# Kernel optimization log

Hardware: AMD Instinct MI355X
Metric: run time of the kernel (lower is better)

The kernel has to match this reference:

```python
import jax, jax.numpy as jnp
import numpy as np

NQ = 4
DIM = 1 << NQ  # 16 statevector amplitudes

def _cnot_perm(c, t):
    idx = np.arange(DIM)
    cbit = (idx >> (NQ - 1 - c)) & 1
    return np.where(cbit == 1, idx ^ (1 << (NQ - 1 - t)), idx)

# BasicEntanglerLayers CNOT ring: (0,1),(1,2),(2,3),(3,0)
CNOT_PERMS = [jnp.asarray(_cnot_perm(q, (q + 1) % NQ)) for q in range(NQ)]
_idx = np.arange(DIM)
SIGNS = jnp.asarray(np.stack([1.0 - 2.0 * ((_idx >> (NQ - 1 - q)) & 1) for q in range(NQ)]).astype(np.float32))  # (NQ, DIM), PauliZ eigenvalues


def _apply_rx(state, theta, q):
    """Apply RX(theta) on wire q. state: (N, DIM) complex64. theta: scalar or (N,)."""
    half = theta * 0.5
    c = jnp.cos(half).astype(jnp.complex64)
    js = (1j * jnp.sin(half)).astype(jnp.complex64)
    if jnp.ndim(theta) == 1:
        c = c[:, None, None]
        js = js[:, None, None]
    d1, d2 = 1 << q, 1 << (NQ - 1 - q)
    st = state.reshape(-1, d1, 2, d2)
    a0, a1 = st[:, :, 0, :], st[:, :, 1, :]
    out = jnp.stack([c * a0 - js * a1, c * a1 - js * a0], axis=2)
    return out.reshape(state.shape)


def circuit(angles, weights):
    """AngleEmbedding(RX) + BasicEntanglerLayers(RX + CNOT ring) + <Z_i>.
    angles: (N, NQ) real. weights: (L, NQ). returns (N, NQ)."""
    N = angles.shape[0]
    state = jnp.zeros((N, DIM), jnp.complex64).at[:, 0].set(1.0)
    for q in range(NQ):  # AngleEmbedding: per-sample RX angles
        state = _apply_rx(state, angles[:, q], q)
    for l in range(weights.shape[0]):  # entangler layers (static count)
        for q in range(NQ):
            state = _apply_rx(state, weights[l, q], q)
        for q in range(NQ):
            state = state[:, CNOT_PERMS[q]]
    probs = jnp.real(state) ** 2 + jnp.imag(state) ** 2
    return probs @ SIGNS.T


def setup_inputs() -> dict:
    key = jax.random.key(0)
    ks = jax.random.split(key, 5)
    B, S = 32, 2048
    TWO_PI = 6.2831853
    return {
        "x": jax.random.normal(ks[0], (B, S, NQ), jnp.float32),
        "weights_Q": jax.random.uniform(ks[1], (1, NQ), jnp.float32) * TWO_PI,
        "weights_K": jax.random.uniform(ks[2], (1, NQ), jnp.float32) * TWO_PI,
        "weights_V": jax.random.uniform(ks[3], (1, NQ), jnp.float32) * TWO_PI,
        "weights_C": jax.random.uniform(ks[4], (1, NQ), jnp.float32) * TWO_PI,
    }


def reference(x, weights_Q, weights_K, weights_V, weights_C):
    B, S, E = x.shape  # E == NQ == 4
    flat = x.reshape(B * S, E)
    Q = circuit(flat, weights_Q).reshape(B, S, E)
    K = circuit(flat, weights_K).reshape(B, S, E)
    V = circuit(flat, weights_V).reshape(B, S, E)
    scores = jnp.einsum('bqe,bke->bqk', Q, K) / (E ** 0.5)
    attn = jax.nn.softmax(scores, axis=-1)
    ctx = jnp.einsum('bqk,bke->bqe', attn, V)
    return circuit(ctx.reshape(B * S, E), weights_C).reshape(B, S, E)
```

## Files before the change

### kernel.cpp

```cpp
#include <hip/hip_runtime.h>

#define DIM 16
#define SEQ 2048


template<int P>
__device__ __forceinline__ void rx_bit(float sr[DIM], float si[DIM], float ch, float sh) {
    constexpr int m = 1 << P;
    #pragma unroll
    for (int i = 0; i < DIM; ++i) {
        if ((i & m) == 0) {
            const int j = i | m;
            float r0 = sr[i], i0 = si[i], r1 = sr[j], i1 = si[j];
            sr[i] = fmaf(ch, r0,  sh * i1);
            si[i] = fmaf(ch, i0, -sh * r1);
            sr[j] = fmaf(ch, r1,  sh * i0);
            si[j] = fmaf(ch, i1, -sh * r0);
        }
    }
}

template<int PC, int PT>
__device__ __forceinline__ void cnot_g(float sr[DIM], float si[DIM]) {
    constexpr int cm = 1 << PC, tm = 1 << PT;
    #pragma unroll
    for (int i = 0; i < DIM; ++i) {
        if ((i & cm) && !(i & tm)) {
            const int j = i | tm;
            float t;
            t = sr[i]; sr[i] = sr[j]; sr[j] = t;
            t = si[i]; si[i] = si[j]; si[j] = t;
        }
    }
}

__device__ __forceinline__ void embed(float sr[DIM], float si[DIM], float4 a) {
    #pragma unroll
    for (int i = 0; i < DIM; ++i) { sr[i] = 0.f; si[i] = 0.f; }
    sr[0] = 1.f;
    float ch, sh;
    __sincosf(0.5f * a.x, &sh, &ch); rx_bit<3>(sr, si, ch, sh);
    __sincosf(0.5f * a.y, &sh, &ch); rx_bit<2>(sr, si, ch, sh);
    __sincosf(0.5f * a.z, &sh, &ch); rx_bit<1>(sr, si, ch, sh);
    __sincosf(0.5f * a.w, &sh, &ch); rx_bit<0>(sr, si, ch, sh);
}

__device__ __forceinline__ void layer(float sr[DIM], float si[DIM], float4 w) {
    float ch, sh;
    __sincosf(0.5f * w.x, &sh, &ch); rx_bit<3>(sr, si, ch, sh);
    __sincosf(0.5f * w.y, &sh, &ch); rx_bit<2>(sr, si, ch, sh);
    __sincosf(0.5f * w.z, &sh, &ch); rx_bit<1>(sr, si, ch, sh);
    __sincosf(0.5f * w.w, &sh, &ch); rx_bit<0>(sr, si, ch, sh);
    cnot_g<3,2>(sr, si);
    cnot_g<2,1>(sr, si);
    cnot_g<1,0>(sr, si);
    cnot_g<0,3>(sr, si);
}

__device__ __forceinline__ float4 measure(const float sr[DIM], const float si[DIM]) {
    float e0 = 0.f, e1 = 0.f, e2 = 0.f, e3 = 0.f;
    #pragma unroll
    for (int i = 0; i < DIM; ++i) {
        float p = fmaf(sr[i], sr[i], si[i] * si[i]);
        e0 += (i & 8) ? -p : p;
        e1 += (i & 4) ? -p : p;
        e2 += (i & 2) ? -p : p;
        e3 += (i & 1) ? -p : p;
    }
    return make_float4(e0, e1, e2, e3);
}


__global__ __launch_bounds__(256) void qkv_kernel(
        const float* __restrict__ x,
        const float* __restrict__ wQp, const float* __restrict__ wKp,
        const float* __restrict__ wVp,
        float4* __restrict__ Q, float4* __restrict__ K, float4* __restrict__ V) {
    const int i = blockIdx.x * 256 + threadIdx.x;
    const float4 xv = ((const float4*)x)[i];
    const float4 wQ = *(const float4*)wQp;
    const float4 wK = *(const float4*)wKp;
    const float4 wV = *(const float4*)wVp;

    float sr[DIM], si[DIM];
    embed(sr, si, xv);

    float tr[DIM], ti[DIM];
    #pragma unroll
    for (int k = 0; k < DIM; ++k) { tr[k] = sr[k]; ti[k] = si[k]; }
    layer(tr, ti, wQ);
    Q[i] = measure(tr, ti);

    #pragma unroll
    for (int k = 0; k < DIM; ++k) { tr[k] = sr[k]; ti[k] = si[k]; }
    layer(tr, ti, wK);
    K[i] = measure(tr, ti);

    layer(sr, si, wV);
    V[i] = measure(sr, si);
}


__global__ __launch_bounds__(256) void attn_kernel(
        const float4* __restrict__ Q, const float4* __restrict__ K,
        const float4* __restrict__ V, const float* __restrict__ wCp,
        float4* __restrict__ out) {
    __shared__ float4 Ks[SEQ];
    __shared__ float4 Vs[SEQ];

    const int b  = blockIdx.x >> 3;
    const int rb = blockIdx.x & 7;

    const float4* Kb = K + b * SEQ;
    const float4* Vb = V + b * SEQ;
    for (int t = threadIdx.x; t < SEQ; t += 256) {
        Ks[t] = Kb[t];
        Vs[t] = Vb[t];
    }
    __syncthreads();

    const int row = b * SEQ + rb * 256 + threadIdx.x;
    const float4 q = Q[row];
    const float qx = q.x * 0.5f, qy = q.y * 0.5f, qz = q.z * 0.5f, qw = q.w * 0.5f;

    float den = 0.f, a0 = 0.f, a1 = 0.f, a2 = 0.f, a3 = 0.f;
    #pragma unroll 8
    for (int k = 0; k < SEQ; ++k) {
        const float4 kv = Ks[k];
        float s = fmaf(qx, kv.x, fmaf(qy, kv.y, fmaf(qz, kv.z, qw * kv.w)));
        float e = __expf(s);
        const float4 vv = Vs[k];
        den += e;
        a0 = fmaf(e, vv.x, a0);
        a1 = fmaf(e, vv.y, a1);
        a2 = fmaf(e, vv.z, a2);
        a3 = fmaf(e, vv.w, a3);
    }
    const float inv = 1.0f / den;
    const float4 ctx = make_float4(a0 * inv, a1 * inv, a2 * inv, a3 * inv);

    const float4 wC = *(const float4*)wCp;
    float sr[DIM], si[DIM];
    embed(sr, si, ctx);
    layer(sr, si, wC);
    out[row] = measure(sr, si);
}


extern "C" void kernel_launch(void* const* d_in, const int* in_sizes, int n_in,
                              void* d_out, int out_size, void* d_ws, size_t ws_size,
                              hipStream_t stream) {
    const float* x  = (const float*)d_in[0];
    const float* wQ = (const float*)d_in[1];
    const float* wK = (const float*)d_in[2];
    const float* wV = (const float*)d_in[3];
    const float* wC = (const float*)d_in[4];

    const int n = in_sizes[0] / 4;
    float4* Q = (float4*)d_ws;
    float4* K = Q + n;
    float4* V = K + n;

    qkv_kernel<<<n / 256, 256, 0, stream>>>(x, wQ, wK, wV, Q, K, V);

    const int batches = n / SEQ;
    attn_kernel<<<batches * 8, 256, 0, stream>>>(Q, K, V, wC, (float4*)d_out);
}
```

Measured before the change: 124.4 us.

## Split attention keys across waves, interleave K/V, parallelize QKV over circuits

The QKV kernel now launches a second grid dimension so each circuit (Q, K, V) runs in its own thread, and K and V are written interleaved. The attention kernel assigns 64 rows per block and splits the 2048 keys into four 512-key chunks, one per wave. K/V are read straight from global memory (wave-uniform broadcast loads) instead of being staged in LDS, and the waves' partial softmax sums are combined through a small shared buffer before the final circuit. The intent is four times as many attention blocks for better occupancy, plus an exp2 with a pre-scaled query. The costs are that the embedding is recomputed three times and that only one wave per block runs the final circuit.

```diff
diff --git a/kernel.cpp b/kernel.cpp
--- a/kernel.cpp
+++ b/kernel.cpp
@@ -2,6 +2,8 @@
 
 #define DIM 16
 #define SEQ 2048
+#define CHUNK 512
+#define ROWS_PER_BLOCK 64
 
 
 template<int P>
@@ -75,75 +77,77 @@
         const float* __restrict__ x,
         const float* __restrict__ wQp, const float* __restrict__ wKp,
         const float* __restrict__ wVp,
-        float4* __restrict__ Q, float4* __restrict__ K, float4* __restrict__ V) {
+        float4* __restrict__ Q, float4* __restrict__ KV, int n) {
     const int i = blockIdx.x * 256 + threadIdx.x;
+    const int which = blockIdx.y;
     const float4 xv = ((const float4*)x)[i];
-    const float4 wQ = *(const float4*)wQp;
-    const float4 wK = *(const float4*)wKp;
-    const float4 wV = *(const float4*)wVp;
+    const float* wp = (which == 0) ? wQp : (which == 1) ? wKp : wVp;
+    const float4 w = *(const float4*)wp;
 
     float sr[DIM], si[DIM];
     embed(sr, si, xv);
+    layer(sr, si, w);
+    const float4 r = measure(sr, si);
 
-    float tr[DIM], ti[DIM];
-    #pragma unroll
-    for (int k = 0; k < DIM; ++k) { tr[k] = sr[k]; ti[k] = si[k]; }
-    layer(tr, ti, wQ);
-    Q[i] = measure(tr, ti);
-
-    #pragma unroll
-    for (int k = 0; k < DIM; ++k) { tr[k] = sr[k]; ti[k] = si[k]; }
-    layer(tr, ti, wK);
-    K[i] = measure(tr, ti);
-
-    layer(sr, si, wV);
-    V[i] = measure(sr, si);
+    if (which == 0)      Q[i]          = r;
+    else if (which == 1) KV[2 * i]     = r;
+    else                 KV[2 * i + 1] = r;
 }
 
 
 __global__ __launch_bounds__(256) void attn_kernel(
-        const float4* __restrict__ Q, const float4* __restrict__ K,
-        const float4* __restrict__ V, const float* __restrict__ wCp,
-        float4* __restrict__ out) {
-    __shared__ float4 Ks[SEQ];
-    __shared__ float4 Vs[SEQ];
+        const float4* __restrict__ Q, const float4* __restrict__ KV,
+        const float* __restrict__ wCp, float4* __restrict__ out) {
+    __shared__ float part[4][ROWS_PER_BLOCK][5];
 
-    const int b  = blockIdx.x >> 3;
-    const int rb = blockIdx.x & 7;
+    const int b    = blockIdx.x >> 5;
+    const int rb   = blockIdx.x & 31;
+    const int wave = threadIdx.x >> 6;
+    const int lane = threadIdx.x & 63;
 
-    const float4* Kb = K + b * SEQ;
-    const float4* Vb = V + b * SEQ;
-    for (int t = threadIdx.x; t < SEQ; t += 256) {
-        Ks[t] = Kb[t];
-        Vs[t] = Vb[t];
-    }
-    __syncthreads();
+    const int row = b * SEQ + rb * ROWS_PER_BLOCK + lane;
+    const float4 q = Q[row];
+    const float SC = 0.72134752044f;
+    const float qx = q.x * SC, qy = q.y * SC, qz = q.z * SC, qw = q.w * SC;
 
-    const int row = b * SEQ + rb * 256 + threadIdx.x;
-    const float4 q = Q[row];
-    const float qx = q.x * 0.5f, qy = q.y * 0.5f, qz = q.z * 0.5f, qw = q.w * 0.5f;
+    const float4* KVb = KV + (size_t)b * (2 * SEQ) + wave * (2 * CHUNK);
 
     float den = 0.f, a0 = 0.f, a1 = 0.f, a2 = 0.f, a3 = 0.f;
     #pragma unroll 8
-    for (int k = 0; k < SEQ; ++k) {
-        const float4 kv = Ks[k];
+    for (int k = 0; k < CHUNK; ++k) {
+        const float4 kv = KVb[2 * k];
+        const float4 vv = KVb[2 * k + 1];
         float s = fmaf(qx, kv.x, fmaf(qy, kv.y, fmaf(qz, kv.z, qw * kv.w)));
-        float e = __expf(s);
-        const float4 vv = Vs[k];
+        float e = exp2f(s);
         den += e;
         a0 = fmaf(e, vv.x, a0);
         a1 = fmaf(e, vv.y, a1);
         a2 = fmaf(e, vv.z, a2);
         a3 = fmaf(e, vv.w, a3);
     }
-    const float inv = 1.0f / den;
-    const float4 ctx = make_float4(a0 * inv, a1 * inv, a2 * inv, a3 * inv);
+    part[wave][lane][0] = den;
+    part[wave][lane][1] = a0;
+    part[wave][lane][2] = a1;
+    part[wave][lane][3] = a2;
+    part[wave][lane][4] = a3;
+    __syncthreads();
 
-    const float4 wC = *(const float4*)wCp;
-    float sr[DIM], si[DIM];
-    embed(sr, si, ctx);
-    layer(sr, si, wC);
-    out[row] = measure(sr, si);
+    if (threadIdx.x < ROWS_PER_BLOCK) {
+        const int r = threadIdx.x;
+        float d  = part[0][r][0] + part[1][r][0] + part[2][r][0] + part[3][r][0];
+        float c0 = part[0][r][1] + part[1][r][1] + part[2][r][1] + part[3][r][1];
+        float c1 = part[0][r][2] + part[1][r][2] + part[2][r][2] + part[3][r][2];
+        float c2 = part[0][r][3] + part[1][r][3] + part[2][r][3] + part[3][r][3];
+        float c3 = part[0][r][4] + part[1][r][4] + part[2][r][4] + part[3][r][4];
+        const float inv = 1.0f / d;
+        const float4 ctx = make_float4(c0 * inv, c1 * inv, c2 * inv, c3 * inv);
+
+        const float4 wC = *(const float4*)wCp;
+        float sr[DIM], si[DIM];
+        embed(sr, si, ctx);
+        layer(sr, si, wC);
+        out[b * SEQ + rb * ROWS_PER_BLOCK + r] = measure(sr, si);
+    }
 }
 
 
@@ -157,12 +161,12 @@
     const float* wC = (const float*)d_in[4];
 
     const int n = in_sizes[0] / 4;
-    float4* Q = (float4*)d_ws;
-    float4* K = Q + n;
-    float4* V = K + n;
+    float4* Q  = (float4*)d_ws;
+    float4* KV = Q + n;
 
-    qkv_kernel<<<n / 256, 256, 0, stream>>>(x, wQ, wK, wV, Q, K, V);
+    dim3 qgrid(n / 256, 3);
+    qkv_kernel<<<qgrid, 256, 0, stream>>>(x, wQ, wK, wV, Q, KV, n);
 
-    const int batches = n / SEQ;
-    attn_kernel<<<batches * 8, 256, 0, stream>>>(Q, K, V, wC, (float4*)d_out);
+    const int blocks = n / ROWS_PER_BLOCK;
+    attn_kernel<<<blocks, 256, 0, stream>>>(Q, KV, wC, (float4*)d_out);
 }
```

Result: slower. 183.4 us (+47.5%).
